# Kernel tuning notes

Measured on AMD Instinct MI355X. Metric: run time of the kernel, lower is better.

Reference implementation:

```python
import jax, jax.numpy as jnp
import numpy as np

N_NODES = 100000


def _gcn_norm(edge_index, edge_weight, n):
    # add self-loops with weight 1 (PyG gcn_norm default fill_value=1.0)
    row = jnp.concatenate([edge_index[0], jnp.arange(n, dtype=edge_index.dtype)])
    col = jnp.concatenate([edge_index[1], jnp.arange(n, dtype=edge_index.dtype)])
    w = jnp.concatenate([edge_weight, jnp.ones((n,), dtype=edge_weight.dtype)])
    deg = jax.ops.segment_sum(w, col, num_segments=n)
    dinv = jnp.where(deg > 0, jax.lax.rsqrt(jnp.where(deg > 0, deg, 1.0)), 0.0)
    norm = dinv[row] * w * dinv[col]  # [E+N]
    return row, col, norm


def _gcn_conv(x, row, col, norm, W, b, n):
    h = x @ W                                   # [N, out] dense projection first (in > out)
    msg = norm[:, None] * h[row]                # gather + scale
    out = jax.ops.segment_sum(msg, col, num_segments=n)  # scatter-add to targets
    return out + b


def setup_inputs() -> dict:
    key = jax.random.key(0)
    ks = jax.random.split(key, 6)
    n, e, f, h, c = N_NODES, 3200000, 256, 64, 40
    return {
        "x": jax.random.normal(ks[0], (n, f), dtype=jnp.float32),
        "edge_index": jax.random.randint(ks[1], (2, e), 0, n, dtype=jnp.int64),
        "edge_weight": jax.random.uniform(ks[2], (e,), dtype=jnp.float32),
        "W1": jax.random.normal(ks[3], (f, h), dtype=jnp.float32) / np.sqrt(f),
        "b1": jnp.zeros((h,), dtype=jnp.float32),
        "W2": jax.random.normal(ks[4], (h, c), dtype=jnp.float32) / np.sqrt(h),
        "b2": jnp.zeros((c,), dtype=jnp.float32),
    }


def reference(x, edge_index, edge_weight, W1, b1, W2, b2):
    n = x.shape[0]
    row, col, norm = _gcn_norm(edge_index, edge_weight, n)
    # layer 1: GCNConv -> identity activation -> dropout (identity at eval)
    h = _gcn_conv(x, row, col, norm, W1, b1, n)
    # layer 2: GCNConv (classifier head)
    out = _gcn_conv(h, row, col, norm, W2, b2, n)
    return out
```

## Files before the change

kernel.cpp:

```cpp
#include <hip/hip_runtime.h>
#include <hip/hip_fp16.h>
#include <cstdint>
#include <cstddef>


#define TB 256
#define NBK 200
#define LCAP 32
#define SPLIT 4
#define GCAP 4096
#define NSL 8

typedef _Float16 half8 __attribute__((ext_vector_type(8)));
typedef float f32x4 __attribute__((ext_vector_type(4)));

__global__ void k_detect(const unsigned* ei, int* flag) {
    int t = threadIdx.x;
    unsigned v = 0;
    for (int i = t; i < 256; i += 64) v |= ei[2 * i + 1];
    unsigned long long any = __ballot(v != 0u);
    if (t == 0) *flag = (any != 0ull) ? 1 : 0;
}

__global__ void k_zero(int* p, int n) {
    int i = blockIdx.x * blockDim.x + threadIdx.x;
    if (i < n) p[i] = 0;
}

__global__ __launch_bounds__(256) void k_binA(const void* __restrict__ ei,
                                              const int* __restrict__ flag,
                                              const float* __restrict__ ew,
                                              int* __restrict__ tail,
                                              int2* __restrict__ stage,
                                              int per, int E, int capx) {
    __shared__ int2 lbuf[NBK][LCAP];
    __shared__ int lcnt[NBK];
    int t = threadIdx.x;
    int myx = blockIdx.x & (NSL - 1);
    for (int i = t; i < NBK; i += 256) lcnt[i] = 0;
    __syncthreads();
    int s0 = blockIdx.x * per;
    int s1 = min(E, s0 + per);
    int isI32 = *flag;
    const int* p32 = (const int*)ei;
    const long long* p64 = (const long long*)ei;
    for (int b0 = s0; b0 < s1; b0 += 2048) {
        int2 ent[8];
        int bk[8];
#pragma unroll
        for (int u = 0; u < 8; u++) {
            int e = b0 + u * 256 + t;
            bk[u] = -1;
            if (e < s1) {
                int r, c;
                if (isI32) { r = p32[e]; c = p32[E + e]; }
                else       { r = (int)p64[e]; c = (int)p64[E + e]; }
                bk[u] = c >> 9;
                ent[u] = make_int2((r << 9) | (c & 511), __float_as_int(ew[e]));
            }
        }
#pragma unroll
        for (int u = 0; u < 8; u++) {
            if (bk[u] < 0) continue;
            int pos = atomicAdd(&lcnt[bk[u]], 1);
            if (pos < LCAP) {
                lbuf[bk[u]][pos] = ent[u];
            } else {
                int slot = bk[u] * NSL + myx;
                int g = atomicAdd(&tail[slot], 1);
                if (g < capx) stage[(size_t)slot * capx + g] = ent[u];
            }
        }
        __syncthreads();
        if (t < NBK) {
            int c = min(lcnt[t], LCAP);
            int n16 = c & ~15;
            if (n16) {
                int slot = t * NSL + myx;
                int base = atomicAdd(&tail[slot], n16);
                size_t db = (size_t)slot * capx;
                for (int j = 0; j < n16; j++) {
                    int g = base + j;
                    if (g < capx) stage[db + g] = lbuf[t][j];
                }
                int rem = c - n16;
                for (int j = 0; j < rem; j++) lbuf[t][j] = lbuf[t][n16 + j];
                lcnt[t] = rem;
            } else {
                lcnt[t] = c;
            }
        }
        __syncthreads();
    }
    if (t < NBK) {
        int c = min(lcnt[t], LCAP);
        if (c) {
            int slot = t * NSL + myx;
            int base = atomicAdd(&tail[slot], c);
            size_t db = (size_t)slot * capx;
            for (int j = 0; j < c; j++) {
                int g = base + j;
                if (g < capx) stage[db + g] = lbuf[t][j];
            }
        }
    }
}

__global__ void k_bscan(const int* __restrict__ tail, int* __restrict__ bbase,
                        int* __restrict__ ptr2, int nbk, int capx, int N) {
    __shared__ int sm[256];
    int t = threadIdx.x;
    int v = 0;
    if (t < nbk)
        for (int x = 0; x < NSL; x++) v += min(tail[t * NSL + x], capx);
    sm[t] = v;
    __syncthreads();
    for (int off = 1; off < 256; off <<= 1) {
        int add = (t >= off) ? sm[t - off] : 0;
        __syncthreads();
        sm[t] += add;
        __syncthreads();
    }
    if (t < nbk) bbase[t] = sm[t] - v;
    if (t == nbk - 1) ptr2[(size_t)N * 4] = sm[t];
}

__global__ __launch_bounds__(512) void k_binB(const int* __restrict__ tail,
                                              const int* __restrict__ bbase,
                                              const int2* __restrict__ stage,
                                              unsigned* __restrict__ csr,
                                              int* __restrict__ ptr2,
                                              float* __restrict__ dinv,
                                              int N, int capx, int qn) {
    __shared__ int h2[2048];
    __shared__ float wsm[512];
    __shared__ int sm[512];
    __shared__ int lpos2[2048];
    __shared__ int cseg[NSL];
    int b = blockIdx.x, t = threadIdx.x;
    for (int i = t; i < 2048; i += 512) h2[i] = 0;
    wsm[t] = 0.f;
    if (t < NSL) cseg[t] = min(tail[b * NSL + t], capx);
    __syncthreads();
#pragma unroll
    for (int x = 0; x < NSL; x++) {
        int m = cseg[x];
        size_t sb = (size_t)(b * NSL + x) * capx;
        for (int j = t; j < m; j += 512) {
            int2 v = stage[sb + j];
            int cl = v.x & 511;
            int src = v.x >> 9;
            int rng = min(src / qn, SPLIT - 1);
            atomicAdd(&h2[(cl << 2) | rng], 1);
            atomicAdd(&wsm[cl], __int_as_float(v.y));
        }
    }
    __syncthreads();
    int a0 = h2[t * 4], a1 = h2[t * 4 + 1], a2 = h2[t * 4 + 2], a3 = h2[t * 4 + 3];
    int s = a0 + a1 + a2 + a3;
    sm[t] = s;
    __syncthreads();
    for (int off = 1; off < 512; off <<= 1) {
        int add = (t >= off) ? sm[t - off] : 0;
        __syncthreads();
        sm[t] += add;
        __syncthreads();
    }
    int ex = sm[t] - s;
    int base = bbase[b];
    int node = b * 512 + t;
    int e0 = ex, e1 = ex + a0, e2 = e1 + a1, e3 = e2 + a2;
    float dv = rsqrtf(1.0f + wsm[t]);
    if (node < N) {
        ptr2[(size_t)node * 4 + 0] = base + e0;
        ptr2[(size_t)node * 4 + 1] = base + e1;
        ptr2[(size_t)node * 4 + 2] = base + e2;
        ptr2[(size_t)node * 4 + 3] = base + e3;
        dinv[node] = dv;
    }
    lpos2[t * 4 + 0] = e0;
    lpos2[t * 4 + 1] = e1;
    lpos2[t * 4 + 2] = e2;
    lpos2[t * 4 + 3] = e3;
    __syncthreads();
    wsm[t] = dv;
    __syncthreads();
#pragma unroll
    for (int x = 0; x < NSL; x++) {
        int m = cseg[x];
        size_t sb = (size_t)(b * NSL + x) * capx;
        for (int j = t; j < m; j += 512) {
            int2 v = stage[sb + j];
            int cl = v.x & 511;
            int src = v.x >> 9;
            int rng = min(src / qn, SPLIT - 1);
            int idx = atomicAdd(&lpos2[(cl << 2) | rng], 1);
            float wfold = __int_as_float(v.y) * wsm[cl];
            unsigned hb = __half_as_ushort(__float2half(wfold)) & 0x7FFFu;
            csr[base + idx] = ((unsigned)src << 15) | hb;
        }
    }
}

__global__ void k_fold(unsigned* __restrict__ csr, const float* __restrict__ dinv,
                       const int* __restrict__ ptr2, int n4) {
    int tot = ptr2[n4];
    int j = blockIdx.x * blockDim.x + threadIdx.x;
    if (j >= tot) return;
    unsigned e = csr[j];
    unsigned r = e >> 15;
    float w = __half2float(__ushort_as_half((unsigned short)(e & 0x7FFFu)));
    float wf = w * dinv[r];
    unsigned hb = __half_as_ushort(__float2half(wf)) & 0x7FFFu;
    csr[j] = (e & ~0x7FFFu) | hb;
}

__global__ void k_wc(const float* __restrict__ W1, const float* __restrict__ b1,
                     const float* __restrict__ W2, __half* __restrict__ Wcf,
                     float* __restrict__ bw) {
    __shared__ float w2s[64 * 40];
    __shared__ __half wcs[256][40];
    int t = threadIdx.x;
    for (int i = t; i < 64 * 40; i += 256) w2s[i] = W2[i];
    __syncthreads();
    float acc[40];
#pragma unroll
    for (int j = 0; j < 40; j++) acc[j] = 0.f;
    for (int k = 0; k < 64; k++) {
        float a = W1[t * 64 + k];
#pragma unroll
        for (int j = 0; j < 40; j++) acc[j] = fmaf(a, w2s[k * 40 + j], acc[j]);
    }
    for (int j = 0; j < 40; j++) wcs[t][j] = __float2half(acc[j]);
    if (t < 40) {
        float accb = 0.f;
        for (int k = 0; k < 64; k++) accb = fmaf(b1[k], w2s[k * 40 + t], accb);
        bw[t] = accb;
    }
    __syncthreads();
    for (int s = 0; s < 48; s++) {
        int o = t * 48 + s;
        int j = o & 7;
        int lane = (o >> 3) & 63;
        int f = o >> 9;
        int nt = f % 3, kt = f / 3;
        int k = kt * 32 + (lane >> 4) * 8 + j;
        int c = nt * 16 + (lane & 15);
        Wcf[o] = (c < 40) ? wcs[k][c] : __float2half(0.f);
    }
}

__global__ __launch_bounds__(256, 2) void k_zmm(const float* __restrict__ x,
                                                const __half* __restrict__ Wcf,
                                                __half* __restrict__ Zh, int n) {
    __shared__ __align__(16) unsigned char xs[128 * 64 * 2];
    int t = threadIdx.x;
    int w = t >> 6;
    int l = t & 63;
    int rlo = l & 15;
    int khi = l >> 4;
    int row0 = blockIdx.x * 128;
    f32x4 acc[2][3];
#pragma unroll
    for (int m = 0; m < 2; m++)
#pragma unroll
        for (int nt = 0; nt < 3; nt++) acc[m][nt] = (f32x4){0.f, 0.f, 0.f, 0.f};

    for (int k0 = 0; k0 < 256; k0 += 64) {
        __syncthreads();
#pragma unroll
        for (int s = 0; s < 8; s++) {
            int i = t + 256 * s;
            int rr = i >> 4;
            int kq = (i & 15) * 4;
            int grow = min(row0 + rr, n - 1);
            float4 v = *(const float4*)&x[(size_t)grow * 256 + k0 + kq];
            __half2 h01 = __floats2half2_rn(v.x, v.y);
            __half2 h23 = __floats2half2_rn(v.z, v.w);
            float2 pk;
            ((__half2*)&pk)[0] = h01;
            ((__half2*)&pk)[1] = h23;
            int byte = (rr * 128 + kq * 2) ^ ((rr & 7) << 4);
            *(float2*)(xs + byte) = pk;
        }
        __syncthreads();
        half8 bfr[2][3];
#pragma unroll
        for (int kt2 = 0; kt2 < 2; kt2++)
#pragma unroll
            for (int nt = 0; nt < 3; nt++) {
                int f = (k0 / 32 + kt2) * 3 + nt;
                bfr[kt2][nt] = *(const half8*)&Wcf[(size_t)(f * 64 + l) * 8];
            }
#pragma unroll
        for (int kt2 = 0; kt2 < 2; kt2++) {
#pragma unroll
            for (int m = 0; m < 2; m++) {
                int row = (w * 2 + m) * 16 + rlo;
                int byte = (row * 128 + kt2 * 64 + khi * 16) ^ ((row & 7) << 4);
                half8 af = *(const half8*)(xs + byte);
#pragma unroll
                for (int nt = 0; nt < 3; nt++)
                    acc[m][nt] = __builtin_amdgcn_mfma_f32_16x16x32_f16(af, bfr[kt2][nt], acc[m][nt], 0, 0, 0);
            }
        }
    }
#pragma unroll
    for (int m = 0; m < 2; m++) {
#pragma unroll
        for (int nt = 0; nt < 3; nt++) {
            int col = nt * 16 + rlo;
            if (col < 40) {
#pragma unroll
                for (int reg = 0; reg < 4; reg++) {
                    int grow = row0 + (w * 2 + m) * 16 + khi * 4 + reg;
                    if (grow < n) Zh[(size_t)grow * 40 + col] = __float2half(acc[m][nt][reg]);
                }
            }
        }
    }
}

template <int MODE>
__global__ __launch_bounds__(320) void k_gather(const int* __restrict__ ptr2,
                                                const unsigned* __restrict__ csr,
                                                const __half* __restrict__ src,
                                                const float* __restrict__ dinv,
                                                const float* __restrict__ bw,
                                                const float* __restrict__ b2,
                                                __half* __restrict__ dsth,
                                                float* __restrict__ dstf, int n) {
    __shared__ unsigned se[GCAP];
    int t = threadIdx.x;
    int ln = t / 5;
    int q = t - ln * 5;
    int c0 = q * 8;
    int n0 = blockIdx.x * 64;
    int node = n0 + ln;
    int n1 = min(n0 + 64, n);
    int st0 = ptr2[(size_t)n0 * 4];
    int en0 = ptr2[(size_t)n1 * 4];
    bool act = (node < n1);
    float d2 = 0.f;
    int st = 0, en = 0;
    float a0 = 0.f, a1 = 0.f, a2 = 0.f, a3 = 0.f, a4 = 0.f, a5 = 0.f, a6 = 0.f, a7 = 0.f;
    float sw = 0.f;
    if (act) {
        float d = dinv[node];
        d2 = d * d;
        st = ptr2[(size_t)node * 4];
        en = ptr2[(size_t)(node + 1) * 4];
        float4 raw = *(const float4*)&src[(size_t)node * 40 + c0];
        const __half2* hh = (const __half2*)&raw;
        float2 f0 = __half22float2(hh[0]), f1 = __half22float2(hh[1]);
        float2 f2 = __half22float2(hh[2]), f3 = __half22float2(hh[3]);
        a0 = d2 * f0.x; a1 = d2 * f0.y; a2 = d2 * f1.x; a3 = d2 * f1.y;
        a4 = d2 * f2.x; a5 = d2 * f2.y; a6 = d2 * f3.x; a7 = d2 * f3.y;
    }
    for (int base = st0; base < en0; base += GCAP) {
        int m = min(GCAP, en0 - base);
        __syncthreads();
        for (int i = t; i < m; i += 320) se[i] = csr[base + i];
        __syncthreads();
        if (act) {
            int lo = max(st, base) - base;
            int hi = min(en, base + m) - base;
#pragma unroll 4
            for (int j = lo; j < hi; j++) {
                unsigned e = se[j];
                float nv = __half2float(__ushort_as_half((unsigned short)(e & 0x7FFFu)));
                unsigned r = e >> 15;
                float4 raw = *(const float4*)&src[(size_t)r * 40 + c0];
                const __half2* hh = (const __half2*)&raw;
                float2 f0 = __half22float2(hh[0]), f1 = __half22float2(hh[1]);
                float2 f2 = __half22float2(hh[2]), f3 = __half22float2(hh[3]);
                if (MODE) sw += nv;
                a0 = fmaf(nv, f0.x, a0); a1 = fmaf(nv, f0.y, a1);
                a2 = fmaf(nv, f1.x, a2); a3 = fmaf(nv, f1.y, a3);
                a4 = fmaf(nv, f2.x, a4); a5 = fmaf(nv, f2.y, a5);
                a6 = fmaf(nv, f3.x, a6); a7 = fmaf(nv, f3.y, a7);
            }
        }
    }
    if (!act) return;
    if (MODE) {
        float sb = sw + d2;
        a0 += sb * bw[c0 + 0] + b2[c0 + 0];
        a1 += sb * bw[c0 + 1] + b2[c0 + 1];
        a2 += sb * bw[c0 + 2] + b2[c0 + 2];
        a3 += sb * bw[c0 + 3] + b2[c0 + 3];
        a4 += sb * bw[c0 + 4] + b2[c0 + 4];
        a5 += sb * bw[c0 + 5] + b2[c0 + 5];
        a6 += sb * bw[c0 + 6] + b2[c0 + 6];
        a7 += sb * bw[c0 + 7] + b2[c0 + 7];
        float4 o0 = make_float4(a0, a1, a2, a3);
        float4 o1 = make_float4(a4, a5, a6, a7);
        *(float4*)&dstf[(size_t)node * 40 + c0] = o0;
        *(float4*)&dstf[(size_t)node * 40 + c0 + 4] = o1;
    } else {
        float4 packed;
        ((__half2*)&packed)[0] = __floats2half2_rn(a0, a1);
        ((__half2*)&packed)[1] = __floats2half2_rn(a2, a3);
        ((__half2*)&packed)[2] = __floats2half2_rn(a4, a5);
        ((__half2*)&packed)[3] = __floats2half2_rn(a6, a7);
        *(float4*)&dsth[(size_t)node * 40 + c0] = packed;
    }
}

extern "C" void kernel_launch(void* const* d_in, const int* in_sizes, int n_in,
                              void* d_out, int out_size, void* d_ws, size_t ws_size,
                              hipStream_t stream) {
    const float* x  = (const float*)d_in[0];
    const void*  ei = d_in[1];
    const float* ew = (const float*)d_in[2];
    const float* W1 = (const float*)d_in[3];
    const float* b1 = (const float*)d_in[4];
    const float* W2 = (const float*)d_in[5];
    const float* b2 = (const float*)d_in[6];
    float* out = (float*)d_out;

    const int E = in_sizes[1] / 2;
    const int N = in_sizes[0] / 256;
    const int nbk = (N + 511) >> 9;
    const int capx = E / (nbk * NSL) + 768;
    const int qn = (N + SPLIT - 1) / SPLIT;

    char* ws = (char*)d_ws;
    float*  dinv = (float*)(ws + 0);
    int*    flag = (int*)(ws + (1u << 19));
    float*  bw   = (float*)(ws + (1u << 19) + 256);
    __half* Wcf  = (__half*)(ws + (1u << 19) + 4096);
    int*    tail = (int*)(ws + (1u << 19) + 65536);
    int*    bbase = (int*)(ws + (1u << 19) + 65536 + 16384);
    size_t off = (size_t)1 << 20;
    size_t estride = ((size_t)E * 4 + 255) & ~(size_t)255;
    size_t n4stride = ((size_t)(N * 4 + 1) * 4 + 255) & ~(size_t)255;
    size_t hstride = ((size_t)N * 40 * 2 + 255) & ~(size_t)255;
    int*      ptr2 = (int*)(ws + off);      off += n4stride;
    unsigned* csr  = (unsigned*)(ws + off); off += estride;
    int2*     stage = (int2*)(ws + off);    off += (size_t)NBK * NSL * capx * 8;
    __half*   Zh   = (__half*)(ws + off);   off += hstride;
    __half*   T1h  = (__half*)(ws + off);

    const int NB = 608;
    const int per = (E + NB - 1) / NB;
    int gb = (N + 63) / 64;

    k_detect<<<1, 64, 0, stream>>>((const unsigned*)ei, flag);
    k_zero<<<(NBK * NSL + TB - 1) / TB, TB, 0, stream>>>(tail, NBK * NSL);
    k_binA<<<NB, 256, 0, stream>>>(ei, flag, ew, tail, stage, per, E, capx);
    k_bscan<<<1, 256, 0, stream>>>(tail, bbase, ptr2, nbk, capx, N);
    k_binB<<<nbk, 512, 0, stream>>>(tail, bbase, stage, csr, ptr2, dinv, N, capx, qn);
    k_fold<<<(E + TB - 1) / TB, TB, 0, stream>>>(csr, dinv, ptr2, N * 4);
    k_wc<<<1, TB, 0, stream>>>(W1, b1, W2, Wcf, bw);
    k_zmm<<<(N + 127) / 128, TB, 0, stream>>>(x, Wcf, Zh, N);
    k_gather<0><<<gb, 320, 0, stream>>>(ptr2, csr, Zh, dinv, bw, b2, T1h, nullptr, N);
    k_gather<1><<<gb, 320, 0, stream>>>(ptr2, csr, T1h, dinv, bw, b2, nullptr, out, N);
}
```

Before: 263.6 us.

## Replace LDS-buffered edge binning with two-pass histogram and reserved-range scatter

The edge binning kernel drops the per-block shared-memory staging buffers with periodic flushes. It now makes two passes over its edge slice: the first builds a per-bucket histogram, the second scatters each edge directly into a global range reserved with one atomic per bucket. This cuts global atomics and the sync-heavy flush loop, at the cost of reading the column indices twice and issuing scattered single-entry writes. The block count is raised so each block handles a smaller slice.

```diff
diff --git a/kernel.cpp b/kernel.cpp
--- a/kernel.cpp
+++ b/kernel.cpp
@@ -6,7 +6,6 @@
 
 #define TB 256
 #define NBK 200
-#define LCAP 32
 #define SPLIT 4
 #define GCAP 4096
 #define NSL 8
@@ -33,76 +32,37 @@
                                               int* __restrict__ tail,
                                               int2* __restrict__ stage,
                                               int per, int E, int capx) {
-    __shared__ int2 lbuf[NBK][LCAP];
-    __shared__ int lcnt[NBK];
+    __shared__ int hist[NBK];
+    __shared__ int rbase[NBK];
+    __shared__ int cur[NBK];
     int t = threadIdx.x;
     int myx = blockIdx.x & (NSL - 1);
-    for (int i = t; i < NBK; i += 256) lcnt[i] = 0;
+    for (int i = t; i < NBK; i += 256) { hist[i] = 0; cur[i] = 0; }
     __syncthreads();
     int s0 = blockIdx.x * per;
     int s1 = min(E, s0 + per);
     int isI32 = *flag;
     const int* p32 = (const int*)ei;
     const long long* p64 = (const long long*)ei;
-    for (int b0 = s0; b0 < s1; b0 += 2048) {
-        int2 ent[8];
-        int bk[8];
-#pragma unroll
-        for (int u = 0; u < 8; u++) {
-            int e = b0 + u * 256 + t;
-            bk[u] = -1;
-            if (e < s1) {
-                int r, c;
-                if (isI32) { r = p32[e]; c = p32[E + e]; }
-                else       { r = (int)p64[e]; c = (int)p64[E + e]; }
-                bk[u] = c >> 9;
-                ent[u] = make_int2((r << 9) | (c & 511), __float_as_int(ew[e]));
-            }
-        }
-#pragma unroll
-        for (int u = 0; u < 8; u++) {
-            if (bk[u] < 0) continue;
-            int pos = atomicAdd(&lcnt[bk[u]], 1);
-            if (pos < LCAP) {
-                lbuf[bk[u]][pos] = ent[u];
-            } else {
-                int slot = bk[u] * NSL + myx;
-                int g = atomicAdd(&tail[slot], 1);
-                if (g < capx) stage[(size_t)slot * capx + g] = ent[u];
-            }
-        }
-        __syncthreads();
-        if (t < NBK) {
-            int c = min(lcnt[t], LCAP);
-            int n16 = c & ~15;
-            if (n16) {
-                int slot = t * NSL + myx;
-                int base = atomicAdd(&tail[slot], n16);
-                size_t db = (size_t)slot * capx;
-                for (int j = 0; j < n16; j++) {
-                    int g = base + j;
-                    if (g < capx) stage[db + g] = lbuf[t][j];
-                }
-                int rem = c - n16;
-                for (int j = 0; j < rem; j++) lbuf[t][j] = lbuf[t][n16 + j];
-                lcnt[t] = rem;
-            } else {
-                lcnt[t] = c;
-            }
-        }
-        __syncthreads();
-    }
-    if (t < NBK) {
-        int c = min(lcnt[t], LCAP);
-        if (c) {
-            int slot = t * NSL + myx;
-            int base = atomicAdd(&tail[slot], c);
-            size_t db = (size_t)slot * capx;
-            for (int j = 0; j < c; j++) {
-                int g = base + j;
-                if (g < capx) stage[db + g] = lbuf[t][j];
-            }
-        }
+    for (int e = s0 + t; e < s1; e += 256) {
+        int c = isI32 ? p32[E + e] : (int)p64[E + e];
+        atomicAdd(&hist[c >> 9], 1);
+    }
+    __syncthreads();
+    for (int i = t; i < NBK; i += 256) {
+        int h = hist[i];
+        rbase[i] = h ? atomicAdd(&tail[i * NSL + myx], h) : 0;
+    }
+    __syncthreads();
+    for (int e = s0 + t; e < s1; e += 256) {
+        int r, c;
+        if (isI32) { r = p32[e]; c = p32[E + e]; }
+        else       { r = (int)p64[e]; c = (int)p64[E + e]; }
+        int bk = c >> 9;
+        int pos = rbase[bk] + atomicAdd(&cur[bk], 1);
+        if (pos < capx)
+            stage[(size_t)(bk * NSL + myx) * capx + pos] =
+                make_int2((r << 9) | (c & 511), __float_as_int(ew[e]));
     }
 }
 
@@ -442,7 +402,7 @@
     __half*   Zh   = (__half*)(ws + off);   off += hstride;
     __half*   T1h  = (__half*)(ws + off);
 
-    const int NB = 608;
+    const int NB = 1024;
     const int per = (E + NB - 1) / NB;
     int gb = (N + 63) / 64;
 
```

Measured after the change: 269.4 us. +2.2%, slower.
